# Performance work log

Hardware: AMD Instinct MI355X
Metric: run time of the kernel (lower is better)

Reference implementation:

```python
import jax, jax.numpy as jnp
import numpy as np

NOPE, ROPE, LORA, VDIM = 128, 64, 512, 128
T, H, S = 1024, 16, 8192
NUM_CHUNKS = 4  # prefix chunks merged via online-softmax LSE combine
SCALING = (NOPE + ROPE) ** -0.5


def setup_inputs() -> dict:
    key = jax.random.key(0)
    k1, k2, k3, k4 = jax.random.split(key, 4)
    q = jax.random.normal(k1, (T, H, NOPE + ROPE), dtype=jnp.float32)
    kv_cache = jax.random.normal(k2, (S, LORA + ROPE), dtype=jnp.float32)  # latent KV cache [S, 576]
    w_kc = jax.random.normal(k3, (H, NOPE, LORA), dtype=jnp.float32) * (NOPE ** -0.5)
    w_vc = jax.random.normal(k4, (H, LORA, VDIM), dtype=jnp.float32) * (LORA ** -0.5)
    return {"q": q, "kv_cache": kv_cache, "w_kc": w_kc, "w_vc": w_vc}


def _chunk_attn(q_full, kv):
    # q_full: [T,H,576], kv chunk: [C,576] (MQA: single latent KV head)
    scores = jnp.einsum('thd,sd->ths', q_full, kv) * SCALING
    lse = jax.nn.logsumexp(scores, axis=-1)               # [T,H]
    p = jnp.exp(scores - lse[..., None])                  # [T,H,C]
    out = jnp.einsum('ths,sl->thl', p, kv[:, :LORA])      # value = latent kv_lora part
    return out, lse


def reference(q, kv_cache, w_kc, w_vc):
    # --- weight-absorbed query projection (forward_absorb) ---
    q_nope, q_pe = q[..., :NOPE], q[..., NOPE:]
    q_lora = jnp.einsum('thn,hnl->thl', q_nope, w_kc)     # bmm(q_nope^T, w_kc)
    q_full = jnp.concatenate([q_lora, q_pe], axis=-1)     # [T,H,576]

    # --- chunked MQA over latent cache with LSE merge (merge_state_v2) ---
    chunks = kv_cache.reshape(NUM_CHUNKS, S // NUM_CHUNKS, LORA + ROPE)
    acc_out, acc_lse = _chunk_attn(q_full, chunks[0])

    def merge(carry, kv):
        a_out, a_lse = carry
        o, lse = _chunk_attn(q_full, kv)
        new_lse = jnp.logaddexp(a_lse, lse)
        new_out = (a_out * jnp.exp(a_lse - new_lse)[..., None]
                   + o * jnp.exp(lse - new_lse)[..., None])
        return (new_out, new_lse), None

    (attn_out, _), _ = jax.lax.scan(merge, (acc_out, acc_lse), chunks[1:])

    # --- weight-absorbed value projection: bmm(attn^T, w_vc) ---
    out = jnp.einsum('thl,hlv->thv', attn_out, w_vc)      # [T,H,128]
    return out.reshape(T, H * VDIM)
```

## Files before the change

### kernel.cpp

```cpp
#include <hip/hip_runtime.h>
#include <stdint.h>
#include <stddef.h>

#define T_TOK 1024
#define NH    16
#define S_KV  8192
#define DQK   576
#define DV    512
#define NROWS (T_TOK*NH)
#define SCALING 0.072168783648703220563f
#define M_FIX 8.0f

#define SC 32
#define NT (S_KV/SC)
#define KV_CH (72*SC)
#define VT_CH (4*DV)

typedef __attribute__((ext_vector_type(8))) short bf16x8;
typedef __attribute__((ext_vector_type(4))) float f32x4;

__device__ __forceinline__ uint16_t f2bf(float f) {
  uint32_t u = __float_as_uint(f);
  u += 0x7FFFu + ((u >> 16) & 1u);
  return (uint16_t)(u >> 16);
}
__device__ __forceinline__ float bf2f(uint16_t v) {
  return __uint_as_float(((uint32_t)v) << 16);
}
__device__ __forceinline__ uint32_t pk2(float a, float b) {
  return (uint32_t)f2bf(a) | ((uint32_t)f2bf(b) << 16);
}
__device__ __forceinline__ void async16(void* lds, const void* g) {
  __builtin_amdgcn_global_load_lds((const __attribute__((address_space(1))) void*)g,
                                   (__attribute__((address_space(3))) void*)lds, 16, 0, 0);
}

__global__ void prep_qfull(const float* __restrict__ q, const float* __restrict__ w_kc,
                           uint16_t* __restrict__ q_full) {
  const int h = blockIdx.y, t0 = blockIdx.x * 32;
  const int tid = threadIdx.x;
  __shared__ float qn[32][128];
  #pragma unroll
  for (int r = 0; r < 4; ++r) {
    int idx4 = r * 256 + tid;
    int row = idx4 >> 5, c4 = (idx4 & 31) * 4;
    const float4 v = *(const float4*)(q + ((size_t)((t0 + row) * NH + h)) * 192 + c4);
    *(float4*)&qn[row][c4] = v;
  }
  __syncthreads();
  const int ty = tid >> 6, tx = tid & 63;
  float acc[8][8];
  #pragma unroll
  for (int i = 0; i < 8; ++i)
    #pragma unroll
    for (int j = 0; j < 8; ++j) acc[i][j] = 0.f;
  for (int n = 0; n < 128; ++n) {
    const float4 b0 = *(const float4*)(w_kc + ((size_t)(h * 128 + n)) * 512 + tx * 8);
    const float4 b1 = *(const float4*)(w_kc + ((size_t)(h * 128 + n)) * 512 + tx * 8 + 4);
    #pragma unroll
    for (int i = 0; i < 8; ++i) {
      const float a = qn[ty * 8 + i][n];
      acc[i][0] += a * b0.x; acc[i][1] += a * b0.y; acc[i][2] += a * b0.z; acc[i][3] += a * b0.w;
      acc[i][4] += a * b1.x; acc[i][5] += a * b1.y; acc[i][6] += a * b1.z; acc[i][7] += a * b1.w;
    }
  }
  #pragma unroll
  for (int i = 0; i < 8; ++i) {
    const size_t R = (size_t)(t0 + ty * 8 + i) * NH + h;
    uint4 o;
    o.x = pk2(acc[i][0]*SCALING, acc[i][1]*SCALING);
    o.y = pk2(acc[i][2]*SCALING, acc[i][3]*SCALING);
    o.z = pk2(acc[i][4]*SCALING, acc[i][5]*SCALING);
    o.w = pk2(acc[i][6]*SCALING, acc[i][7]*SCALING);
    *(uint4*)&q_full[R * DQK + tx * 8] = o;
  }
  {
    const int trow = tid >> 3, j0 = (tid & 7) * 8;
    const float* src = q + ((size_t)((t0 + trow) * NH + h)) * 192 + 128 + j0;
    const float4 a = *(const float4*)(src);
    const float4 b = *(const float4*)(src + 4);
    const size_t R = (size_t)(t0 + trow) * NH + h;
    uint4 o;
    o.x = pk2(a.x*SCALING, a.y*SCALING); o.y = pk2(a.z*SCALING, a.w*SCALING);
    o.z = pk2(b.x*SCALING, b.y*SCALING); o.w = pk2(b.z*SCALING, b.w*SCALING);
    *(uint4*)&q_full[R * DQK + 512 + j0] = o;
  }
}

__global__ void prep_kv(const float* __restrict__ kv, uint16_t* __restrict__ kv_t,
                        uint16_t* __restrict__ vt_t) {
  const int st = blockIdx.x, tid = threadIdx.x;
  uint16_t* kvo = kv_t + (size_t)st * (KV_CH * 8);
  #pragma unroll
  for (int r = 0; r < 9; ++r) {
    const int k = r * 256 + tid;
    const int dc = k >> 5, sl = k & 31;
    const float* src = kv + ((size_t)(st * SC + sl)) * DQK + dc * 8;
    const float4 a = *(const float4*)src;
    const float4 b = *(const float4*)(src + 4);
    uint4 o;
    o.x = pk2(a.x, a.y); o.y = pk2(a.z, a.w); o.z = pk2(b.x, b.y); o.w = pk2(b.z, b.w);
    *(uint4*)&kvo[(size_t)k * 8] = o;
  }
  uint16_t* vto = vt_t + (size_t)st * (VT_CH * 8);
  #pragma unroll
  for (int r = 0; r < 8; ++r) {
    const int k = r * 256 + tid;
    const int sc = k >> 9, v = k & 511;
    float val[8];
    #pragma unroll
    for (int e = 0; e < 8; ++e)
      val[e] = kv[((size_t)(st * SC + sc * 8 + e)) * DQK + v];
    uint4 o;
    o.x = pk2(val[0], val[1]); o.y = pk2(val[2], val[3]);
    o.z = pk2(val[4], val[5]); o.w = pk2(val[6], val[7]);
    *(uint4*)&vto[(size_t)k * 8] = o;
  }
}

__global__ __launch_bounds__(768, 3) void attn_kernel(
    const uint16_t* __restrict__ q_full, const uint16_t* __restrict__ kv_t,
    const uint16_t* __restrict__ vt_t, uint16_t* __restrict__ attn_o) {
  __shared__ short kv_lds[2][KV_CH * 8];
  __shared__ short P_lds[2][260 * 8];
  __shared__ float l_sh[64];

  const int tid = threadIdx.x;
  const int wv = tid >> 6, lane = tid & 63;
  const int cc = lane & 15, quad = lane >> 4;
  const int R0 = blockIdx.x * 64;

  if (wv < 4) {
    const int qh = wv & 1, sh = wv >> 1;
    bf16x8 qf[2][18];
    #pragma unroll
    for (int j = 0; j < 2; ++j) {
      const uint16_t* qrow = q_full + (size_t)(R0 + 32 * qh + 16 * j + cc) * DQK + quad * 8;
      #pragma unroll
      for (int kk = 0; kk < 18; ++kk)
        qf[j][kk] = *(const bf16x8*)(qrow + kk * 32);
    }
    const int sc0 = 2 * sh + (cc >> 3), e = cc & 7;
    const int qb0 = 32 * qh + quad * 4, qb1 = qb0 + 16;

    for (int st = 0; st <= NT; ++st) {
      __syncthreads();
      if (st < NT) {
        const short* kb = kv_lds[st & 1];
        f32x4 sa0 = {0.f,0.f,0.f,0.f}, sa1 = {0.f,0.f,0.f,0.f};
        #pragma unroll
        for (int kk = 0; kk < 18; ++kk) {
          const bf16x8 b0 = *(const bf16x8*)&kb[((kk * 4 + quad) * SC + sh * 16 + cc) * 8];
          sa0 = __builtin_amdgcn_mfma_f32_16x16x32_bf16(qf[0][kk], b0, sa0, 0, 0, 0);
          sa1 = __builtin_amdgcn_mfma_f32_16x16x32_bf16(qf[1][kk], b0, sa1, 0, 0, 0);
        }
        short* Pb = P_lds[st & 1];
        #pragma unroll
        for (int r = 0; r < 4; ++r) {
          Pb[(sc0 * 65 + qb0 + r) * 8 + e] = (short)f2bf(__expf(sa0[r] - M_FIX));
          Pb[(sc0 * 65 + qb1 + r) * 8 + e] = (short)f2bf(__expf(sa1[r] - M_FIX));
        }
      }
    }
    __syncthreads();
  } else {
    const int ci = wv - 4;
    f32x4 acc[4][4];
    #pragma unroll
    for (int a = 0; a < 4; ++a)
      #pragma unroll
      for (int b = 0; b < 4; ++b) acc[a][b] = (f32x4){0.f, 0.f, 0.f, 0.f};
    f32x4 accl[4];
    #pragma unroll
    for (int a = 0; a < 4; ++a) accl[a] = (f32x4){0.f, 0.f, 0.f, 0.f};
    bf16x8 ones;
    #pragma unroll
    for (int e2 = 0; e2 < 8; ++e2) ones[e2] = (short)0x3F80;

    {
      const uint16_t* kt = kv_t;
      #pragma unroll
      for (int r = 0; r < 5; ++r) {
        const int base = r * 512 + ci * 64;
        if (base < KV_CH)
          async16(&kv_lds[0][base * 8], kt + (size_t)(base + lane) * 8);
      }
    }

    for (int st = 0; st <= NT; ++st) {
      __syncthreads();
      if (st + 1 < NT) {
        const uint16_t* kt = kv_t + (size_t)(st + 1) * (KV_CH * 8);
        short* dst = kv_lds[(st + 1) & 1];
        #pragma unroll
        for (int r = 0; r < 5; ++r) {
          const int base = r * 512 + ci * 64;
          if (base < KV_CH)
            async16(&dst[base * 8], kt + (size_t)(base + lane) * 8);
        }
      }
      if (st > 0) {
        const short* Pb = P_lds[(st - 1) & 1];
        bf16x8 af[4];
        #pragma unroll
        for (int q2 = 0; q2 < 4; ++q2)
          af[q2] = *(const bf16x8*)&Pb[(quad * 65 + 16 * q2 + cc) * 8];
        const uint16_t* vtile = vt_t + (size_t)(st - 1) * (VT_CH * 8);
        bf16x8 vt4[4];
        #pragma unroll
        for (int vj = 0; vj < 4; ++vj)
          vt4[vj] = *(const bf16x8*)(vtile + (size_t)(quad * 512 + 64 * ci + 16 * vj + cc) * 8);
        if (ci == 0) {
          #pragma unroll
          for (int q2 = 0; q2 < 4; ++q2)
            accl[q2] = __builtin_amdgcn_mfma_f32_16x16x32_bf16(af[q2], ones, accl[q2], 0, 0, 0);
        }
        #pragma unroll
        for (int q2 = 0; q2 < 4; ++q2)
          #pragma unroll
          for (int vj = 0; vj < 4; ++vj)
            acc[q2][vj] = __builtin_amdgcn_mfma_f32_16x16x32_bf16(af[q2], vt4[vj], acc[q2][vj], 0, 0, 0);
      }
    }
    if (ci == 0 && cc == 0) {
      #pragma unroll
      for (int q2 = 0; q2 < 4; ++q2)
        #pragma unroll
        for (int r = 0; r < 4; ++r)
          l_sh[16 * q2 + quad * 4 + r] = accl[q2][r];
    }
    __syncthreads();
    #pragma unroll
    for (int q2 = 0; q2 < 4; ++q2) {
      #pragma unroll
      for (int r = 0; r < 4; ++r) {
        const int row = 16 * q2 + quad * 4 + r;
        const float li = 1.0f / l_sh[row];
        #pragma unroll
        for (int vj = 0; vj < 4; ++vj)
          attn_o[(size_t)(R0 + row) * DV + 64 * ci + 16 * vj + cc] = f2bf(acc[q2][vj][r] * li);
      }
    }
  }
}

__global__ void out_proj(const uint16_t* __restrict__ attn_o, const float* __restrict__ w_vc,
                         float* __restrict__ out) {
  const int h = blockIdx.y, t0 = blockIdx.x * 32;
  const int tid = threadIdx.x;
  __shared__ uint16_t at[32 * 512];
  #pragma unroll
  for (int r = 0; r < 8; ++r) {
    const int idx = r * 256 + tid;
    const int row = idx >> 6, c8 = (idx & 63) * 8;
    const uint4 v = *(const uint4*)&attn_o[((size_t)((t0 + row) * NH + h)) * DV + c8];
    *(uint4*)&at[row * 512 + c8] = v;
  }
  __syncthreads();
  const int tx = tid & 31, ty = tid >> 5;
  float4 a0 = {0,0,0,0}, a1 = {0,0,0,0}, a2 = {0,0,0,0}, a3 = {0,0,0,0};
  const uint16_t* r0 = &at[(ty * 4 + 0) * 512];
  const uint16_t* r1 = &at[(ty * 4 + 1) * 512];
  const uint16_t* r2 = &at[(ty * 4 + 2) * 512];
  const uint16_t* r3 = &at[(ty * 4 + 3) * 512];
  for (int l = 0; l < 512; ++l) {
    const float4 b = *(const float4*)(w_vc + ((size_t)h * 512 + l) * 128 + tx * 4);
    const float x0 = bf2f(r0[l]), x1 = bf2f(r1[l]);
    const float x2 = bf2f(r2[l]), x3 = bf2f(r3[l]);
    a0.x += x0 * b.x; a0.y += x0 * b.y; a0.z += x0 * b.z; a0.w += x0 * b.w;
    a1.x += x1 * b.x; a1.y += x1 * b.y; a1.z += x1 * b.z; a1.w += x1 * b.w;
    a2.x += x2 * b.x; a2.y += x2 * b.y; a2.z += x2 * b.z; a2.w += x2 * b.w;
    a3.x += x3 * b.x; a3.y += x3 * b.y; a3.z += x3 * b.z; a3.w += x3 * b.w;
  }
  const size_t orow = (size_t)(NH * 128);
  float* o0 = out + (size_t)(t0 + ty * 4) * orow + h * 128 + tx * 4;
  *(float4*)(o0)            = a0;
  *(float4*)(o0 + orow)     = a1;
  *(float4*)(o0 + 2 * orow) = a2;
  *(float4*)(o0 + 3 * orow) = a3;
}

extern "C" void kernel_launch(void* const* d_in, const int* in_sizes, int n_in,
                              void* d_out, int out_size, void* d_ws, size_t ws_size,
                              hipStream_t stream) {
  const float* q    = (const float*)d_in[0];
  const float* kv   = (const float*)d_in[1];
  const float* w_kc = (const float*)d_in[2];
  const float* w_vc = (const float*)d_in[3];
  float* out = (float*)d_out;

  char* ws = (char*)d_ws;
  const size_t SZ_QF = (size_t)NROWS * DQK * 2;
  const size_t SZ_KT = (size_t)NT * KV_CH * 16;
  const size_t SZ_VT = (size_t)NT * VT_CH * 16;
  uint16_t* q_full = (uint16_t*)(ws);
  uint16_t* kv_t   = (uint16_t*)(ws + SZ_QF);
  uint16_t* vt_t   = (uint16_t*)(ws + SZ_QF + SZ_KT);
  uint16_t* attn_o = (uint16_t*)(ws + SZ_QF + SZ_KT + SZ_VT);

  prep_qfull<<<dim3(32, 16), 256, 0, stream>>>(q, w_kc, q_full);
  prep_kv<<<NT, 256, 0, stream>>>(kv, kv_t, vt_t);
  attn_kernel<<<256, 768, 0, stream>>>(q_full, kv_t, vt_t, attn_o);
  out_proj<<<dim3(32, 16), 256, 0, stream>>>(attn_o, w_vc, out);
}
```

Before: 444.4 us.

## Move output projection to bf16 MFMA and hoist V-tile global loads

Replaces the scalar fp32 FMA output projection with a bf16 MFMA kernel. A new prep kernel repacks w_vc into a bf16 layout laid out for MFMA B-operands. Separately, the attention loop now issues the V-tile global loads at the start of each iteration, ahead of the K prefetch and P reads, to hide their latency. This adds an extra launch and a bf16 rounding of w_vc, which slightly reduces accuracy.

```diff
diff --git a/kernel.cpp b/kernel.cpp
--- a/kernel.cpp
+++ b/kernel.cpp
@@ -23,9 +23,6 @@
   uint32_t u = __float_as_uint(f);
   u += 0x7FFFu + ((u >> 16) & 1u);
   return (uint16_t)(u >> 16);
-}
-__device__ __forceinline__ float bf2f(uint16_t v) {
-  return __uint_as_float(((uint32_t)v) << 16);
 }
 __device__ __forceinline__ uint32_t pk2(float a, float b) {
   return (uint32_t)f2bf(a) | ((uint32_t)f2bf(b) << 16);
@@ -118,6 +115,20 @@
   }
 }
 
+__global__ void wvt_prep(const float* __restrict__ w_vc, uint16_t* __restrict__ wvt) {
+  const int c = blockIdx.x * 256 + threadIdx.x;
+  const int h = c >> 13, rem = c & 8191;
+  const int lc = rem >> 7, v = rem & 127;
+  const float* src = w_vc + ((size_t)h * 512 + lc * 8) * 128 + v;
+  float val[8];
+  #pragma unroll
+  for (int e = 0; e < 8; ++e) val[e] = src[e * 128];
+  uint4 o;
+  o.x = pk2(val[0], val[1]); o.y = pk2(val[2], val[3]);
+  o.z = pk2(val[4], val[5]); o.w = pk2(val[6], val[7]);
+  *(uint4*)&wvt[(size_t)c * 8] = o;
+}
+
 __global__ __launch_bounds__(768, 3) void attn_kernel(
     const uint16_t* __restrict__ q_full, const uint16_t* __restrict__ kv_t,
     const uint16_t* __restrict__ vt_t, uint16_t* __restrict__ attn_o) {
@@ -189,6 +200,13 @@
 
     for (int st = 0; st <= NT; ++st) {
       __syncthreads();
+      bf16x8 vt4[4];
+      if (st > 0) {
+        const uint16_t* vtile = vt_t + (size_t)(st - 1) * (VT_CH * 8);
+        #pragma unroll
+        for (int vj = 0; vj < 4; ++vj)
+          vt4[vj] = *(const bf16x8*)(vtile + (size_t)(quad * 512 + 64 * ci + 16 * vj + cc) * 8);
+      }
       if (st + 1 < NT) {
         const uint16_t* kt = kv_t + (size_t)(st + 1) * (KV_CH * 8);
         short* dst = kv_lds[(st + 1) & 1];
@@ -205,11 +223,6 @@
         #pragma unroll
         for (int q2 = 0; q2 < 4; ++q2)
           af[q2] = *(const bf16x8*)&Pb[(quad * 65 + 16 * q2 + cc) * 8];
-        const uint16_t* vtile = vt_t + (size_t)(st - 1) * (VT_CH * 8);
-        bf16x8 vt4[4];
-        #pragma unroll
-        for (int vj = 0; vj < 4; ++vj)
-          vt4[vj] = *(const bf16x8*)(vtile + (size_t)(quad * 512 + 64 * ci + 16 * vj + cc) * 8);
         if (ci == 0) {
           #pragma unroll
           for (int q2 = 0; q2 < 4; ++q2)
@@ -244,40 +257,33 @@
   }
 }
 
-__global__ void out_proj(const uint16_t* __restrict__ attn_o, const float* __restrict__ w_vc,
-                         float* __restrict__ out) {
-  const int h = blockIdx.y, t0 = blockIdx.x * 32;
-  const int tid = threadIdx.x;
-  __shared__ uint16_t at[32 * 512];
-  #pragma unroll
-  for (int r = 0; r < 8; ++r) {
-    const int idx = r * 256 + tid;
-    const int row = idx >> 6, c8 = (idx & 63) * 8;
-    const uint4 v = *(const uint4*)&attn_o[((size_t)((t0 + row) * NH + h)) * DV + c8];
-    *(uint4*)&at[row * 512 + c8] = v;
-  }
-  __syncthreads();
-  const int tx = tid & 31, ty = tid >> 5;
-  float4 a0 = {0,0,0,0}, a1 = {0,0,0,0}, a2 = {0,0,0,0}, a3 = {0,0,0,0};
-  const uint16_t* r0 = &at[(ty * 4 + 0) * 512];
-  const uint16_t* r1 = &at[(ty * 4 + 1) * 512];
-  const uint16_t* r2 = &at[(ty * 4 + 2) * 512];
-  const uint16_t* r3 = &at[(ty * 4 + 3) * 512];
-  for (int l = 0; l < 512; ++l) {
-    const float4 b = *(const float4*)(w_vc + ((size_t)h * 512 + l) * 128 + tx * 4);
-    const float x0 = bf2f(r0[l]), x1 = bf2f(r1[l]);
-    const float x2 = bf2f(r2[l]), x3 = bf2f(r3[l]);
-    a0.x += x0 * b.x; a0.y += x0 * b.y; a0.z += x0 * b.z; a0.w += x0 * b.w;
-    a1.x += x1 * b.x; a1.y += x1 * b.y; a1.z += x1 * b.z; a1.w += x1 * b.w;
-    a2.x += x2 * b.x; a2.y += x2 * b.y; a2.z += x2 * b.z; a2.w += x2 * b.w;
-    a3.x += x3 * b.x; a3.y += x3 * b.y; a3.z += x3 * b.z; a3.w += x3 * b.w;
-  }
-  const size_t orow = (size_t)(NH * 128);
-  float* o0 = out + (size_t)(t0 + ty * 4) * orow + h * 128 + tx * 4;
-  *(float4*)(o0)            = a0;
-  *(float4*)(o0 + orow)     = a1;
-  *(float4*)(o0 + 2 * orow) = a2;
-  *(float4*)(o0 + 3 * orow) = a3;
+__global__ __launch_bounds__(256) void out_proj(const uint16_t* __restrict__ attn_o,
+                                                const uint16_t* __restrict__ wvt,
+                                                float* __restrict__ out) {
+  const int h = blockIdx.y, t0 = blockIdx.x * 64;
+  const int wv = threadIdx.x >> 6, lane = threadIdx.x & 63;
+  const int cc = lane & 15, quad = lane >> 4;
+
+  f32x4 acc[8];
+  #pragma unroll
+  for (int vj = 0; vj < 8; ++vj) acc[vj] = (f32x4){0.f, 0.f, 0.f, 0.f};
+
+  const uint16_t* arow = attn_o + ((size_t)(t0 + wv * 16 + cc) * NH + h) * DV + quad * 8;
+  const uint16_t* wb = wvt + (size_t)h * (64 * 128) * 8;
+  #pragma unroll 4
+  for (int kk = 0; kk < 16; ++kk) {
+    const bf16x8 a = *(const bf16x8*)(arow + kk * 32);
+    #pragma unroll
+    for (int vj = 0; vj < 8; ++vj) {
+      const bf16x8 b = *(const bf16x8*)(wb + (size_t)(((kk * 4 + quad) * 128) + 16 * vj + cc) * 8);
+      acc[vj] = __builtin_amdgcn_mfma_f32_16x16x32_bf16(a, b, acc[vj], 0, 0, 0);
+    }
+  }
+  #pragma unroll
+  for (int vj = 0; vj < 8; ++vj)
+    #pragma unroll
+    for (int r = 0; r < 4; ++r)
+      out[(size_t)(t0 + wv * 16 + quad * 4 + r) * (NH * 128) + h * 128 + 16 * vj + cc] = acc[vj][r];
 }
 
 extern "C" void kernel_launch(void* const* d_in, const int* in_sizes, int n_in,
@@ -293,13 +299,16 @@
   const size_t SZ_QF = (size_t)NROWS * DQK * 2;
   const size_t SZ_KT = (size_t)NT * KV_CH * 16;
   const size_t SZ_VT = (size_t)NT * VT_CH * 16;
+  const size_t SZ_AO = (size_t)NROWS * DV * 2;
   uint16_t* q_full = (uint16_t*)(ws);
   uint16_t* kv_t   = (uint16_t*)(ws + SZ_QF);
   uint16_t* vt_t   = (uint16_t*)(ws + SZ_QF + SZ_KT);
   uint16_t* attn_o = (uint16_t*)(ws + SZ_QF + SZ_KT + SZ_VT);
+  uint16_t* wvt    = (uint16_t*)(ws + SZ_QF + SZ_KT + SZ_VT + SZ_AO);
 
   prep_qfull<<<dim3(32, 16), 256, 0, stream>>>(q, w_kc, q_full);
   prep_kv<<<NT, 256, 0, stream>>>(kv, kv_t, vt_t);
+  wvt_prep<<<512, 256, 0, stream>>>(w_vc, wvt);
   attn_kernel<<<256, 768, 0, stream>>>(q_full, kv_t, vt_t, attn_o);
-  out_proj<<<dim3(32, 16), 256, 0, stream>>>(attn_o, w_vc, out);
-}
+  out_proj<<<dim3(16, 16), 256, 0, stream>>>(attn_o, wvt, out);
+}
```

Result: faster. 422.8 us (-4.9%).
